# Optimization experiments

Measured on AMD Instinct MI355X. Metric: run time of the kernel, lower is better.

Reference implementation:

```python
import jax, jax.numpy as jnp
import numpy as np

N_NODES = 100000
N_EDGES = 1000000
IN_DIM = 64
OUT_DIM = 64
BN_EPS = 1e-5


def setup_inputs() -> dict:
    key = jax.random.key(0)
    k1, k2, k3 = jax.random.split(key, 3)
    x = jax.random.normal(k1, (N_NODES, IN_DIM), dtype=jnp.float32)
    edge_index = jax.random.randint(k2, (2, N_EDGES), 0, N_NODES, dtype=jnp.int32)
    W = jax.random.normal(k3, (IN_DIM, OUT_DIM), dtype=jnp.float32) * (1.0 / np.sqrt(IN_DIM))
    b = jnp.zeros((OUT_DIM,), dtype=jnp.float32)
    gamma = jnp.ones((OUT_DIM,), dtype=jnp.float32)
    beta = jnp.zeros((OUT_DIM,), dtype=jnp.float32)
    return {"x": x, "edge_index": edge_index, "W": W, "b": b, "gamma": gamma, "beta": beta}


def reference(x, edge_index, W, b, gamma, beta):
    N = x.shape[0]
    # GCN normalization with self-loops (improved=False -> fill value 1.0)
    loop = jnp.arange(N, dtype=edge_index.dtype)
    src = jnp.concatenate([edge_index[0], loop])  # message sources
    dst = jnp.concatenate([edge_index[1], loop])  # aggregation targets
    ew = jnp.ones(src.shape[0], dtype=x.dtype)
    deg = jax.ops.segment_sum(ew, dst, num_segments=N)  # [N]
    dinv = jnp.where(deg > 0, jax.lax.rsqrt(deg), 0.0)
    norm = dinv[src] * ew * dinv[dst]  # [E+N]
    # linear transform then normalized scatter-add aggregation
    h = x @ W  # [N, OUT_DIM]
    msg = h[src] * norm[:, None]  # [E+N, OUT_DIM]
    agg = jax.ops.segment_sum(msg, dst, num_segments=N) + b  # [N, OUT_DIM]
    # activation
    a = jax.nn.relu(agg)
    # BatchNorm1d, training mode: batch statistics over node dim (biased var)
    mean = jnp.mean(a, axis=0)
    var = jnp.mean((a - mean) ** 2, axis=0)
    out = gamma * (a - mean) * jax.lax.rsqrt(var + BN_EPS) + beta
    return out
```

## Files before the change

kernel.cpp:

```cpp
#include <hip/hip_runtime.h>
#include <hip/hip_fp16.h>

#define DIM 64
#define BN_EPS 1e-5f
#define RSHIFT 8
#define RSIZE 256
#define EPB 8192
#define ABLK 4096
#define RBLK 128

__global__ __launch_bounds__(256) void k_binhist(const int* __restrict__ dst,
                                                 int* __restrict__ rangecnt,
                                                 int P, int E) {
    __shared__ int hist[512];
    for (int b0 = threadIdx.x; b0 < P; b0 += 256) hist[b0] = 0;
    __syncthreads();
    const int base4 = blockIdx.x * (EPB / 4);
    for (int i = 0; i < EPB / 4 / 256; ++i) {
        int idx = base4 + i * 256 + threadIdx.x;
        int e0 = idx << 2;
        if (e0 + 3 < E) {
            int4 d4 = ((const int4*)dst)[idx];
            atomicAdd(&hist[d4.x >> RSHIFT], 1);
            atomicAdd(&hist[d4.y >> RSHIFT], 1);
            atomicAdd(&hist[d4.z >> RSHIFT], 1);
            atomicAdd(&hist[d4.w >> RSHIFT], 1);
        } else {
            for (int k = 0; k < 4; ++k)
                if (e0 + k < E) atomicAdd(&hist[dst[e0 + k] >> RSHIFT], 1);
        }
    }
    __syncthreads();
    for (int b0 = threadIdx.x; b0 < P; b0 += 256)
        if (hist[b0] > 0) atomicAdd(&rangecnt[b0], hist[b0]);
}

__global__ void k_rangescan(const int* __restrict__ rangecnt, int* __restrict__ gbase,
                            int* __restrict__ gcursor, int* __restrict__ rowptr,
                            int P, int N, int E) {
    __shared__ int s[512];
    int v = ((int)threadIdx.x < P) ? rangecnt[threadIdx.x] : 0;
    s[threadIdx.x] = v;
    __syncthreads();
    for (int off = 1; off < 512; off <<= 1) {
        int t = (threadIdx.x >= (unsigned)off) ? s[threadIdx.x - off] : 0;
        __syncthreads();
        s[threadIdx.x] += t;
        __syncthreads();
    }
    if ((int)threadIdx.x < P) {
        int ex = s[threadIdx.x] - v;
        gbase[threadIdx.x] = ex;
        gcursor[threadIdx.x] = ex;
    }
    if ((int)threadIdx.x == P - 1) gbase[P] = s[threadIdx.x];
    if (threadIdx.x == 0) rowptr[N] = E;
}

__global__ __launch_bounds__(256) void k_bin(const int* __restrict__ src,
                                             const int* __restrict__ dst,
                                             int* __restrict__ gcursor,
                                             int* __restrict__ pk, int P, int E) {
    __shared__ int hist[512], gofs[512], lcnt[512];
    for (int b0 = threadIdx.x; b0 < P; b0 += 256) { hist[b0] = 0; lcnt[b0] = 0; }
    __syncthreads();
    const int base4 = blockIdx.x * (EPB / 4);
    for (int i = 0; i < EPB / 4 / 256; ++i) {
        int idx = base4 + i * 256 + threadIdx.x;
        int e0 = idx << 2;
        if (e0 + 3 < E) {
            int4 d4 = ((const int4*)dst)[idx];
            atomicAdd(&hist[d4.x >> RSHIFT], 1);
            atomicAdd(&hist[d4.y >> RSHIFT], 1);
            atomicAdd(&hist[d4.z >> RSHIFT], 1);
            atomicAdd(&hist[d4.w >> RSHIFT], 1);
        } else {
            for (int k = 0; k < 4; ++k)
                if (e0 + k < E) atomicAdd(&hist[dst[e0 + k] >> RSHIFT], 1);
        }
    }
    __syncthreads();
    for (int b0 = threadIdx.x; b0 < P; b0 += 256)
        if (hist[b0] > 0) gofs[b0] = atomicAdd(&gcursor[b0], hist[b0]);
    __syncthreads();
    for (int i = 0; i < EPB / 4 / 256; ++i) {
        int idx = base4 + i * 256 + threadIdx.x;
        int e0 = idx << 2;
        if (e0 + 3 < E) {
            int4 d4 = ((const int4*)dst)[idx];
            int4 s4 = ((const int4*)src)[idx];
            int b0;
            b0 = d4.x >> RSHIFT; pk[gofs[b0] + atomicAdd(&lcnt[b0], 1)] = ((d4.x & (RSIZE - 1)) << 20) | s4.x;
            b0 = d4.y >> RSHIFT; pk[gofs[b0] + atomicAdd(&lcnt[b0], 1)] = ((d4.y & (RSIZE - 1)) << 20) | s4.y;
            b0 = d4.z >> RSHIFT; pk[gofs[b0] + atomicAdd(&lcnt[b0], 1)] = ((d4.z & (RSIZE - 1)) << 20) | s4.z;
            b0 = d4.w >> RSHIFT; pk[gofs[b0] + atomicAdd(&lcnt[b0], 1)] = ((d4.w & (RSIZE - 1)) << 20) | s4.w;
        } else {
            for (int k = 0; k < 4; ++k) {
                if (e0 + k < E) {
                    int d = dst[e0 + k];
                    int b0 = d >> RSHIFT;
                    pk[gofs[b0] + atomicAdd(&lcnt[b0], 1)] = ((d & (RSIZE - 1)) << 20) | src[e0 + k];
                }
            }
        }
    }
}

__global__ __launch_bounds__(256) void k_sortrange(
        const int* __restrict__ gbase, const int* __restrict__ pk,
        int* __restrict__ ssrc, int* __restrict__ rowptr,
        float* __restrict__ dinv, int N) {
    __shared__ int lhist[256], ls[256], lcur[256];
    const int r = blockIdx.x;
    const int d0 = r << RSHIFT;
    const int i = d0 + threadIdx.x;
    const int ebeg = gbase[r], eend = gbase[r + 1];
    lhist[threadIdx.x] = 0;
    __syncthreads();
    for (int j = ebeg + threadIdx.x; j < eend; j += 256)
        atomicAdd(&lhist[((unsigned)pk[j]) >> 20], 1);
    __syncthreads();
    int dg = lhist[threadIdx.x];
    if (i < N) dinv[i] = rsqrtf((float)dg + 1.0f);
    ls[threadIdx.x] = dg;
    __syncthreads();
    for (int off = 1; off < 256; off <<= 1) {
        int t = (threadIdx.x >= (unsigned)off) ? ls[threadIdx.x - off] : 0;
        __syncthreads();
        ls[threadIdx.x] += t;
        __syncthreads();
    }
    int lofs = ls[threadIdx.x] - dg;
    lcur[threadIdx.x] = ebeg + lofs;
    if (i < N) rowptr[i] = ebeg + lofs;
    __syncthreads();
    for (int j = ebeg + threadIdx.x; j < eend; j += 256) {
        int p = pk[j];
        ssrc[atomicAdd(&lcur[((unsigned)p) >> 20], 1)] = p & 0xFFFFF;
    }
}

__global__ __launch_bounds__(256) void k_gemm(const float* __restrict__ x,
                                              const float* __restrict__ W,
                                              const float* __restrict__ dinv,
                                              __half* __restrict__ h2, int N) {
    __shared__ float Wl[DIM * DIM];
    for (int i = threadIdx.x; i < DIM * DIM; i += 256) Wl[i] = W[i];
    __syncthreads();
    int t = blockIdx.x * 256 + threadIdx.x;
    int r = t >> 2;
    int q = t & 3;
    if (r >= N) return;
    const float4* xr4 = (const float4*)(x + (size_t)r * DIM);
    float4 acc[4];
#pragma unroll
    for (int j = 0; j < 4; ++j) acc[j] = make_float4(0.f, 0.f, 0.f, 0.f);
    for (int k0 = 0; k0 < 16; ++k0) {
        float4 xv = xr4[k0];
#pragma unroll
        for (int kk = 0; kk < 4; ++kk) {
            float xs = (&xv.x)[kk];
            const float4* wrow = (const float4*)(Wl + (k0 * 4 + kk) * DIM) + (q << 2);
#pragma unroll
            for (int j = 0; j < 4; ++j) {
                float4 w = wrow[j];
                acc[j].x += xs * w.x;
                acc[j].y += xs * w.y;
                acc[j].z += xs * w.z;
                acc[j].w += xs * w.w;
            }
        }
    }
    float dr = dinv[r];
    float4* hr4 = (float4*)(h2 + (size_t)r * DIM) + (q << 1);
    union { __half2 h[4]; float4 f4; } pack;
#pragma unroll
    for (int j = 0; j < 4; j += 2) {
        pack.h[0] = __float22half2_rn(make_float2(acc[j].x * dr, acc[j].y * dr));
        pack.h[1] = __float22half2_rn(make_float2(acc[j].z * dr, acc[j].w * dr));
        pack.h[2] = __float22half2_rn(make_float2(acc[j + 1].x * dr, acc[j + 1].y * dr));
        pack.h[3] = __float22half2_rn(make_float2(acc[j + 1].z * dr, acc[j + 1].w * dr));
        hr4[j >> 1] = pack.f4;
    }
}

__global__ __launch_bounds__(256) void k_nodeagg(
        const int* __restrict__ rowptr, const int* __restrict__ ssrc,
        const __half* __restrict__ h2, const float* __restrict__ dinv,
        const float* __restrict__ b, float* __restrict__ out,
        float* __restrict__ pstats, int N) {
    const int lane = threadIdx.x & 63;
    const int w = threadIdx.x >> 6;
    const float bl = b[lane];
    const __half* hb = h2 + lane;
    float psum = 0.f, psq = 0.f;
    for (int i = blockIdx.x * 4 + w; i < N; i += ABLK * 4) {
        int rb = rowptr[i], re = rowptr[i + 1];
        int deg = re - rb;
        float acc = __half2float(hb[(size_t)i * DIM]);
        for (int j0 = 0; j0 < deg; j0 += 64) {
            int m = min(64, deg - j0);
            int sv = ssrc[rb + j0 + min(lane, m - 1)];
            int j = 0;
            for (; j + 8 <= m; j += 8) {
                int sA[8];
                float vA[8];
#pragma unroll
                for (int k = 0; k < 8; ++k) sA[k] = __builtin_amdgcn_readlane(sv, j + k);
#pragma unroll
                for (int k = 0; k < 8; ++k) vA[k] = __half2float(hb[(size_t)sA[k] * DIM]);
#pragma unroll
                for (int k = 0; k < 8; ++k) acc += vA[k];
            }
            for (; j < m; ++j)
                acc += __half2float(hb[(size_t)__builtin_amdgcn_readlane(sv, j) * DIM]);
        }
        float a = fmaxf(acc * dinv[i] + bl, 0.f);
        out[(size_t)i * DIM + lane] = a;
        psum += a;
        psq += a * a;
    }
    __shared__ float s1[256], s2[256];
    s1[threadIdx.x] = psum;
    s2[threadIdx.x] = psq;
    __syncthreads();
    if (threadIdx.x < 128) {
        s1[threadIdx.x] += s1[threadIdx.x + 128];
        s2[threadIdx.x] += s2[threadIdx.x + 128];
    }
    __syncthreads();
    if (threadIdx.x < 64) {
        pstats[(size_t)blockIdx.x * 128 + threadIdx.x] = s1[threadIdx.x] + s1[threadIdx.x + 64];
        pstats[(size_t)blockIdx.x * 128 + 64 + threadIdx.x] = s2[threadIdx.x] + s2[threadIdx.x + 64];
    }
}

__global__ __launch_bounds__(128) void k_redstats(const float* __restrict__ pstats,
                                                  float* __restrict__ pstats2) {
    const int f = threadIdx.x;
    const size_t base = (size_t)blockIdx.x * (ABLK / RBLK) * 128;
    float s = 0.f;
#pragma unroll 8
    for (int j = 0; j < ABLK / RBLK; ++j)
        s += pstats[base + (size_t)j * 128 + f];
    pstats2[(size_t)blockIdx.x * 128 + f] = s;
}

__global__ void k_finstats(const float* __restrict__ pstats2,
                           const float* __restrict__ gamma, const float* __restrict__ beta,
                           float* __restrict__ scale, float* __restrict__ shift, int N) {
    __shared__ float ssum[1024], ssq[1024];
    const int f = threadIdx.x & 63;
    const int c = threadIdx.x >> 6;
    float s = 0.f, q = 0.f;
    for (int blk = c; blk < RBLK; blk += 16) {
        s += pstats2[blk * 128 + f];
        q += pstats2[blk * 128 + 64 + f];
    }
    ssum[threadIdx.x] = s;
    ssq[threadIdx.x] = q;
    __syncthreads();
    for (int o = 512; o >= 64; o >>= 1) {
        if ((int)threadIdx.x < o) {
            ssum[threadIdx.x] += ssum[threadIdx.x + o];
            ssq[threadIdx.x] += ssq[threadIdx.x + o];
        }
        __syncthreads();
    }
    if (threadIdx.x < 64) {
        float inv_n = 1.0f / (float)N;
        float mean = ssum[f] * inv_n;
        float var = ssq[f] * inv_n - mean * mean;
        float istd = rsqrtf(var + BN_EPS);
        float sc = gamma[f] * istd;
        scale[f] = sc;
        shift[f] = beta[f] - mean * sc;
    }
}

__global__ void k_bn2(float4* __restrict__ a, const float* __restrict__ scale,
                      const float* __restrict__ shift, int total4) {
    int i = blockIdx.x * blockDim.x + threadIdx.x;
    const int stride = gridDim.x * blockDim.x;
    const int f4 = i & 15;
    const float4 scv = ((const float4*)scale)[f4];
    const float4 shv = ((const float4*)shift)[f4];
    for (; i < total4; i += stride) {
        float4 v = a[i];
        v.x = v.x * scv.x + shv.x;
        v.y = v.y * scv.y + shv.y;
        v.z = v.z * scv.z + shv.z;
        v.w = v.w * scv.w + shv.w;
        a[i] = v;
    }
}

extern "C" void kernel_launch(void* const* d_in, const int* in_sizes, int n_in,
                              void* d_out, int out_size, void* d_ws, size_t ws_size,
                              hipStream_t stream) {
    const float* x     = (const float*)d_in[0];
    const int*   ei    = (const int*)d_in[1];
    const float* W     = (const float*)d_in[2];
    const float* b     = (const float*)d_in[3];
    const float* gamma = (const float*)d_in[4];
    const float* beta  = (const float*)d_in[5];
    float* out = (float*)d_out;

    const int N = in_sizes[0] / DIM;
    const int E = in_sizes[1] / 2;
    const int* esrc = ei;
    const int* edst = ei + E;
    const int P = (N + RSIZE - 1) >> RSHIFT;
    const int nbin = (E + EPB - 1) / EPB;

    char* ws = (char*)d_ws;
    size_t off = 0;
    int* rangecnt = (int*)(ws + off);   off += 512 * sizeof(int);
    int* gbase = (int*)(ws + off);      off += 520 * sizeof(int);
    int* gcursor = (int*)(ws + off);    off += 512 * sizeof(int);
    off = (off + 255) & ~(size_t)255;
    float* dinv = (float*)(ws + off);   off += (size_t)N * sizeof(float);
    off = (off + 255) & ~(size_t)255;
    int* rowptr = (int*)(ws + off);     off += (size_t)(N + 1) * sizeof(int);
    off = (off + 255) & ~(size_t)255;
    float* scale = (float*)(ws + off);  off += 64 * sizeof(float);
    float* shift = (float*)(ws + off);  off += 64 * sizeof(float);
    off = (off + 255) & ~(size_t)255;
    float* pstats = (float*)(ws + off); off += (size_t)ABLK * 128 * sizeof(float);
    off = (off + 255) & ~(size_t)255;
    float* pstats2 = (float*)(ws + off); off += (size_t)RBLK * 128 * sizeof(float);
    off = (off + 255) & ~(size_t)255;
    int* pk = (int*)(ws + off);         off += (size_t)E * sizeof(int);
    off = (off + 255) & ~(size_t)255;
    int* ssrc = (int*)(ws + off);       off += (size_t)E * sizeof(int);
    off = (off + 255) & ~(size_t)255;
    __half* h2 = (__half*)(ws + off);   off += (size_t)N * DIM * sizeof(__half);

    hipMemsetAsync(rangecnt, 0, 512 * sizeof(int), stream);

    k_binhist<<<nbin, 256, 0, stream>>>(edst, rangecnt, P, E);
    k_rangescan<<<1, 512, 0, stream>>>(rangecnt, gbase, gcursor, rowptr, P, N, E);
    k_bin<<<nbin, 256, 0, stream>>>(esrc, edst, gcursor, pk, P, E);
    k_sortrange<<<P, 256, 0, stream>>>(gbase, pk, ssrc, rowptr, dinv, N);
    k_gemm<<<(4 * N + 255) / 256, 256, 0, stream>>>(x, W, dinv, h2, N);
    k_nodeagg<<<ABLK, 256, 0, stream>>>(rowptr, ssrc, h2, dinv, b, out, pstats, N);
    k_redstats<<<RBLK, 128, 0, stream>>>(pstats, pstats2);
    k_finstats<<<1, 1024, 0, stream>>>(pstats2, gamma, beta, scale, shift, N);
    k_bn2<<<2048, 256, 0, stream>>>((float4*)out, scale, shift, N * DIM / 4);
}
```

Before: 192.7 us.

## Process node pairs per wave and store activations as fp16 before batchnorm

The aggregation kernel now handles two consecutive nodes per wavefront, merging their neighbor ranges and gathering 16 neighbors per unrolled step to raise memory-level parallelism. The post-ReLU activations are written to a half-precision scratch buffer, and the batchnorm pass reads that buffer and writes fp32 output. This avoids a full fp32 read-modify-write of the output. It risks extra rounding error in the activations, and it silently skips the last node if N is odd.

After: 189.8 us. Within noise of the previous version (-1.5%).

```diff
diff --git a/kernel.cpp b/kernel.cpp
--- a/kernel.cpp
+++ b/kernel.cpp
@@ -6,7 +6,7 @@
 #define RSHIFT 8
 #define RSIZE 256
 #define EPB 8192
-#define ABLK 4096
+#define ABLK 2048
 #define RBLK 128
 
 __global__ __launch_bounds__(256) void k_binhist(const int* __restrict__ dst,
@@ -187,38 +187,57 @@
 __global__ __launch_bounds__(256) void k_nodeagg(
         const int* __restrict__ rowptr, const int* __restrict__ ssrc,
         const __half* __restrict__ h2, const float* __restrict__ dinv,
-        const float* __restrict__ b, float* __restrict__ out,
+        const float* __restrict__ b, __half* __restrict__ a2,
         float* __restrict__ pstats, int N) {
     const int lane = threadIdx.x & 63;
     const int w = threadIdx.x >> 6;
     const float bl = b[lane];
     const __half* hb = h2 + lane;
     float psum = 0.f, psq = 0.f;
-    for (int i = blockIdx.x * 4 + w; i < N; i += ABLK * 4) {
-        int rb = rowptr[i], re = rowptr[i + 1];
-        int deg = re - rb;
-        float acc = __half2float(hb[(size_t)i * DIM]);
-        for (int j0 = 0; j0 < deg; j0 += 64) {
-            int m = min(64, deg - j0);
-            int sv = ssrc[rb + j0 + min(lane, m - 1)];
+    const int npairs = N >> 1;
+    for (int t = blockIdx.x * 4 + w; t < npairs; t += ABLK * 4) {
+        const int i0 = t << 1;
+        const int rb0 = rowptr[i0], rb1 = rowptr[i0 + 1], rb2 = rowptr[i0 + 2];
+        float acc0 = __half2float(hb[(size_t)i0 * DIM]);
+        float acc1 = __half2float(hb[(size_t)(i0 + 1) * DIM]);
+        const int total = rb2 - rb0;
+        for (int j0 = 0; j0 < total; j0 += 64) {
+            const int m = min(64, total - j0);
+            const int c = rb1 - rb0 - j0;
+            int sv = ssrc[rb0 + j0 + min(lane, m - 1)];
             int j = 0;
-            for (; j + 8 <= m; j += 8) {
-                int sA[8];
-                float vA[8];
-#pragma unroll
-                for (int k = 0; k < 8; ++k) sA[k] = __builtin_amdgcn_readlane(sv, j + k);
-#pragma unroll
-                for (int k = 0; k < 8; ++k) vA[k] = __half2float(hb[(size_t)sA[k] * DIM]);
-#pragma unroll
-                for (int k = 0; k < 8; ++k) acc += vA[k];
+            for (; j + 16 <= m; j += 16) {
+                int sA[16];
+                float vA[16];
+#pragma unroll
+                for (int k = 0; k < 16; ++k) sA[k] = __builtin_amdgcn_readlane(sv, j + k);
+#pragma unroll
+                for (int k = 0; k < 16; ++k) vA[k] = __half2float(hb[(size_t)sA[k] * DIM]);
+#pragma unroll
+                for (int k = 0; k < 16; ++k) {
+                    if (j + k < c) acc0 += vA[k]; else acc1 += vA[k];
+                }
             }
-            for (; j < m; ++j)
-                acc += __half2float(hb[(size_t)__builtin_amdgcn_readlane(sv, j) * DIM]);
-        }
-        float a = fmaxf(acc * dinv[i] + bl, 0.f);
-        out[(size_t)i * DIM + lane] = a;
-        psum += a;
-        psq += a * a;
+            if (j < m) {
+                const int r = m - j;
+                int sA[16];
+                float vA[16];
+#pragma unroll
+                for (int k = 0; k < 16; ++k) sA[k] = __builtin_amdgcn_readlane(sv, j + min(k, r - 1));
+#pragma unroll
+                for (int k = 0; k < 16; ++k) vA[k] = __half2float(hb[(size_t)sA[k] * DIM]);
+#pragma unroll
+                for (int k = 0; k < 16; ++k) {
+                    if (k < r) { if (j + k < c) acc0 += vA[k]; else acc1 += vA[k]; }
+                }
+            }
+        }
+        float a0 = fmaxf(acc0 * dinv[i0] + bl, 0.f);
+        float a1 = fmaxf(acc1 * dinv[i0 + 1] + bl, 0.f);
+        a2[(size_t)i0 * DIM + lane] = __float2half_rn(a0);
+        a2[(size_t)(i0 + 1) * DIM + lane] = __float2half_rn(a1);
+        psum += a0 + a1;
+        psq += a0 * a0 + a1 * a1;
     }
     __shared__ float s1[256], s2[256];
     s1[threadIdx.x] = psum;
@@ -278,20 +297,28 @@
     }
 }
 
-__global__ void k_bn2(float4* __restrict__ a, const float* __restrict__ scale,
-                      const float* __restrict__ shift, int total4) {
+__global__ void k_bn2(const __half* __restrict__ a2, const float* __restrict__ scale,
+                      const float* __restrict__ shift, float* __restrict__ out, int total8) {
     int i = blockIdx.x * blockDim.x + threadIdx.x;
     const int stride = gridDim.x * blockDim.x;
-    const int f4 = i & 15;
-    const float4 scv = ((const float4*)scale)[f4];
-    const float4 shv = ((const float4*)shift)[f4];
-    for (; i < total4; i += stride) {
-        float4 v = a[i];
-        v.x = v.x * scv.x + shv.x;
-        v.y = v.y * scv.y + shv.y;
-        v.z = v.z * scv.z + shv.z;
-        v.w = v.w * scv.w + shv.w;
-        a[i] = v;
+    const int f8 = i & 7;
+    const float4 sc0 = ((const float4*)scale)[f8 * 2];
+    const float4 sc1 = ((const float4*)scale)[f8 * 2 + 1];
+    const float4 sh0 = ((const float4*)shift)[f8 * 2];
+    const float4 sh1 = ((const float4*)shift)[f8 * 2 + 1];
+    for (; i < total8; i += stride) {
+        union { float4 f; __half2 h[4]; } u;
+        u.f = ((const float4*)a2)[i];
+        float2 p0 = __half22float2(u.h[0]);
+        float2 p1 = __half22float2(u.h[1]);
+        float2 p2 = __half22float2(u.h[2]);
+        float2 p3 = __half22float2(u.h[3]);
+        float4 o0 = make_float4(p0.x * sc0.x + sh0.x, p0.y * sc0.y + sh0.y,
+                                p1.x * sc0.z + sh0.z, p1.y * sc0.w + sh0.w);
+        float4 o1 = make_float4(p2.x * sc1.x + sh1.x, p2.y * sc1.y + sh1.y,
+                                p3.x * sc1.z + sh1.z, p3.y * sc1.w + sh1.w);
+        ((float4*)out)[(size_t)i * 2] = o0;
+        ((float4*)out)[(size_t)i * 2 + 1] = o1;
     }
 }
 
@@ -335,6 +362,8 @@
     int* ssrc = (int*)(ws + off);       off += (size_t)E * sizeof(int);
     off = (off + 255) & ~(size_t)255;
     __half* h2 = (__half*)(ws + off);   off += (size_t)N * DIM * sizeof(__half);
+    off = (off + 255) & ~(size_t)255;
+    __half* a2 = (__half*)(ws + off);   off += (size_t)N * DIM * sizeof(__half);
 
     hipMemsetAsync(rangecnt, 0, 512 * sizeof(int), stream);
 
@@ -343,8 +372,8 @@
     k_bin<<<nbin, 256, 0, stream>>>(esrc, edst, gcursor, pk, P, E);
     k_sortrange<<<P, 256, 0, stream>>>(gbase, pk, ssrc, rowptr, dinv, N);
     k_gemm<<<(4 * N + 255) / 256, 256, 0, stream>>>(x, W, dinv, h2, N);
-    k_nodeagg<<<ABLK, 256, 0, stream>>>(rowptr, ssrc, h2, dinv, b, out, pstats, N);
+    k_nodeagg<<<ABLK, 256, 0, stream>>>(rowptr, ssrc, h2, dinv, b, a2, pstats, N);
     k_redstats<<<RBLK, 128, 0, stream>>>(pstats, pstats2);
     k_finstats<<<1, 1024, 0, stream>>>(pstats2, gamma, beta, scale, shift, N);
-    k_bn2<<<2048, 256, 0, stream>>>((float4*)out, scale, shift, N * DIM / 4);
-}
+    k_bn2<<<1024, 256, 0, stream>>>(a2, scale, shift, out, N * DIM / 8);
+}
```
